# Kernel optimization log

Measured on AMD Instinct MI355X. Metric: run time of the kernel, lower is better.

The kernel has to match this reference:

```python
import jax, jax.numpy as jnp
import numpy as np

T, B, NINP, NHID, NOUT = 512, 256, 128, 512, 64


def setup_inputs() -> dict:
    key = jax.random.key(0)
    ks = jax.random.split(key, 8)
    s = 0.05
    return {
        "input": jax.random.normal(ks[0], (T, B, NINP - 1), dtype=jnp.float32),
        "dt": jax.random.uniform(ks[1], (T, B, 1), dtype=jnp.float32),
        "W_ih": jax.random.normal(ks[2], (4 * NHID, NINP), dtype=jnp.float32) * s,
        "W_hh": jax.random.normal(ks[3], (4 * NHID, NHID), dtype=jnp.float32) * s,
        "b_ih": jax.random.normal(ks[4], (4 * NHID,), dtype=jnp.float32) * s,
        "b_hh": jax.random.normal(ks[5], (4 * NHID,), dtype=jnp.float32) * s,
        "W_cls": jax.random.normal(ks[6], (NOUT, NHID), dtype=jnp.float32) * s,
        "b_cls": jax.random.normal(ks[7], (NOUT,), dtype=jnp.float32) * s,
    }


def reference(input, dt, W_ih, W_hh, b_ih, b_hh, W_cls, b_cls):
    # x_t = cat(inp_t, dt_t) -> [T, B, NINP]
    x = jnp.concatenate([input, dt], axis=-1)
    nhid = W_hh.shape[1]
    # Precompute input projections for all steps: [T, B, 4*nhid]
    x_proj = jnp.einsum("tbi,gi->tbg", x, W_ih) + b_ih + b_hh

    def step(carry, xp_t):
        h, c = carry
        gates = xp_t + h @ W_hh.T  # [B, 4*nhid]
        i, f, g, o = jnp.split(gates, 4, axis=-1)  # PyTorch LSTMCell gate order
        i = jax.nn.sigmoid(i)
        f = jax.nn.sigmoid(f)
        g = jnp.tanh(g)
        o = jax.nn.sigmoid(o)
        c = f * c + i * g
        h = o * jnp.tanh(c)
        return (h, c), h

    h0 = jnp.zeros((x.shape[1], nhid), dtype=x.dtype)
    c0 = jnp.zeros((x.shape[1], nhid), dtype=x.dtype)
    _, hs = jax.lax.scan(step, (h0, c0), x_proj)  # hs: [T, B, nhid]
    out = jnp.einsum("tbh,oh->tbo", hs, W_cls) + b_cls  # [T, B, nout]
    return out
```

## Files before the change

kernel.cpp:

```cpp
#include <hip/hip_runtime.h>
#include <stdint.h>

#define TT 512
#define BB 256
#define HH 512
#define NOUTC 64

typedef _Float16 f16;
typedef f16 f16x8 __attribute__((ext_vector_type(8)));
typedef float f32x4 __attribute__((ext_vector_type(4)));
typedef unsigned long long ull;

__device__ __forceinline__ float sigmoidf_(float x) {
  x = fminf(fmaxf(x, -30.f), 30.f);
  return 1.f / (1.f + __expf(-x));
}
__device__ __forceinline__ float tanhf_(float x) {
  x = fminf(fmaxf(x, -15.f), 15.f);
  float e = __expf(2.f * x);
  return (e - 1.f) / (e + 1.f);
}

__device__ __forceinline__ f16x8 cvt8(const float* __restrict__ src) {
  float4 p0 = *(const float4*)(src);
  float4 p1 = *(const float4*)(src + 4);
  f16x8 a;
  a[0] = (f16)p0.x; a[1] = (f16)p0.y; a[2] = (f16)p0.z; a[3] = (f16)p0.w;
  a[4] = (f16)p1.x; a[5] = (f16)p1.y; a[6] = (f16)p1.z; a[7] = (f16)p1.w;
  return a;
}

__global__ void zero_ws(uint32_t* __restrict__ ws, int nws) {
  int idx = blockIdx.x * blockDim.x + threadIdx.x;
  int stride = gridDim.x * blockDim.x;
  for (int i = idx; i < nws; i += stride) ws[i] = 0u;
}

__global__ __launch_bounds__(256, 1) void lstm_kernel(
    const float* __restrict__ input, const float* __restrict__ dtp,
    const float* __restrict__ W_ih, const float* __restrict__ W_hh,
    const float* __restrict__ b_ih, const float* __restrict__ b_hh,
    const float* __restrict__ W_cls, const float* __restrict__ b_cls,
    float* __restrict__ out, f16* __restrict__ h_buf) {
  __shared__ __align__(16) f16 xh_h[2][16][520];
  __shared__ __align__(16) f16 xb[2][16][136];
  __shared__ __align__(16) f16x8 wlds[16][64];

  const int tid = threadIdx.x;
  const int g = blockIdx.x & 15;
  const int s = blockIdx.x >> 4;
  const int b0 = g * 16;
  const int w = tid >> 6;
  const int lane = tid & 63;
  const int l = lane & 15;
  const int quad = lane >> 4;
  const int mt_o = s & 3;
  const bool cls_block = (s < 4);
  const int hb = s * 32 + w * 8;

  f16x8 afrag[2][20];
#pragma unroll
  for (int mp = 0; mp < 2; ++mp) {
    const int grow = (mp * 2 + (l >> 3)) * HH + hb + (l & 7);
#pragma unroll
    for (int it = 0; it < 20; ++it) {
      const int kb = it * 32 + quad * 8;
      const float* src = (kb < 128) ? (W_ih + (size_t)grow * 128 + kb)
                                    : (W_hh + (size_t)grow * HH + (kb - 128));
      afrag[mp][it] = cvt8(src);
    }
  }

  float gb_i[4], gb_f[4], gb_g[4], gb_o[4];
  {
    const int hg = hb + (quad & 1) * 4;
#pragma unroll
    for (int r = 0; r < 4; ++r) {
      gb_i[r] = b_ih[0 * HH + hg + r] + b_hh[0 * HH + hg + r];
      gb_f[r] = b_ih[1 * HH + hg + r] + b_hh[1 * HH + hg + r];
      gb_g[r] = b_ih[2 * HH + hg + r] + b_hh[2 * HH + hg + r];
      gb_o[r] = b_ih[3 * HH + hg + r] + b_hh[3 * HH + hg + r];
    }
  }

  float bcls4[4] = {0.f, 0.f, 0.f, 0.f};
  if (cls_block && w == 0) {
#pragma unroll
    for (int r = 0; r < 4; ++r) bcls4[r] = b_cls[mt_o * 16 + quad * 4 + r];
#pragma unroll
    for (int it = 0; it < 16; ++it)
      wlds[it][lane] =
          cvt8(W_cls + (size_t)(mt_o * 16 + l) * HH + it * 32 + quad * 8);
  }

  auto classify = [&](int slot, int tt) {
    f32x4 oa = {0.f, 0.f, 0.f, 0.f}, ob = {0.f, 0.f, 0.f, 0.f};
#pragma unroll
    for (int it = 0; it < 16; it += 2) {
      f16x8 ba = *(const f16x8*)(&xh_h[slot][l][it * 32 + quad * 8]);
      f16x8 bb = *(const f16x8*)(&xh_h[slot][l][(it + 1) * 32 + quad * 8]);
      oa = __builtin_amdgcn_mfma_f32_16x16x32_f16(wlds[it][lane], ba, oa, 0, 0, 0);
      ob = __builtin_amdgcn_mfma_f32_16x16x32_f16(wlds[it + 1][lane], bb, ob, 0, 0, 0);
    }
    float4 o;
    o.x = oa[0] + ob[0] + bcls4[0];
    o.y = oa[1] + ob[1] + bcls4[1];
    o.z = oa[2] + ob[2] + bcls4[2];
    o.w = oa[3] + ob[3] + bcls4[3];
    *(float4*)(out + ((size_t)tt * BB + b0 + l) * NOUTC + mt_o * 16 +
               quad * 4) = o;
  };

  auto stage_h = [&](int t_) {
    const uint32_t e = (uint32_t)((((t_ - 1) >> 1) & 1) ^ 1);
    const ull* hbp =
        (const ull*)h_buf + ((size_t)((t_ - 1) & 1) * 16 + g) * 2048;
    ull v[8];
#pragma unroll
    for (int ci = 0; ci < 8; ++ci)
      v[ci] = __hip_atomic_load(hbp + ci * 256 + tid, __ATOMIC_RELAXED,
                                __HIP_MEMORY_SCOPE_AGENT);
    for (int spin = 0; spin < (1 << 16); ++spin) {
      uint32_t stale = 0;
#pragma unroll
      for (int ci = 0; ci < 8; ++ci)
        if (((uint32_t)v[ci] ^ e) & 1u) stale |= 1u << ci;
      if (!stale) break;
      __builtin_amdgcn_s_sleep(1);
#pragma unroll
      for (int ci = 0; ci < 8; ++ci)
        if (stale & (1u << ci))
          v[ci] = __hip_atomic_load(hbp + ci * 256 + tid, __ATOMIC_RELAXED,
                                    __HIP_MEMORY_SCOPE_AGENT);
    }
#pragma unroll
    for (int ci = 0; ci < 8; ++ci) {
      const int c2 = ci * 256 + tid;
      *(ull*)(&xh_h[t_ & 1][c2 >> 7][(c2 & 127) * 4]) = v[ci];
    }
  };

  {
    ull* zp = (ull*)&xh_h[0][0][0];
    for (int i = tid; i < 2080; i += 256) zp[i] = 0ull;
  }
  const int kx = tid & 127;
  const int nx0 = tid >> 7;
  float xf[8];
#pragma unroll
  for (int ii = 0; ii < 8; ++ii) {
    const int row = b0 + ii * 2 + nx0;
    xf[ii] = (kx < 127) ? input[(size_t)row * 127 + kx] : dtp[row];
  }
  float cc[4] = {0.f, 0.f, 0.f, 0.f};

  for (int t = 0; t < TT; ++t) {
    if (t > 0) stage_h(t);

#pragma unroll
    for (int ii = 0; ii < 8; ++ii) xb[t & 1][ii * 2 + nx0][kx] = (f16)xf[ii];

    __syncthreads();

    f32x4 acc0 = {0.f, 0.f, 0.f, 0.f}, acc1 = {0.f, 0.f, 0.f, 0.f};
    const int xs = t & 1;
#pragma unroll
    for (int it = 0; it < 4; ++it) {
      f16x8 b = *(const f16x8*)(&xb[xs][l][it * 32 + quad * 8]);
      acc0 = __builtin_amdgcn_mfma_f32_16x16x32_f16(afrag[0][it], b, acc0, 0, 0, 0);
      acc1 = __builtin_amdgcn_mfma_f32_16x16x32_f16(afrag[1][it], b, acc1, 0, 0, 0);
    }
#pragma unroll
    for (int kk = 0; kk < 16; ++kk) {
      f16x8 b = *(const f16x8*)(&xh_h[xs][l][kk * 32 + quad * 8]);
      acc0 = __builtin_amdgcn_mfma_f32_16x16x32_f16(afrag[0][4 + kk], b, acc0, 0, 0, 0);
      acc1 = __builtin_amdgcn_mfma_f32_16x16x32_f16(afrag[1][4 + kk], b, acc1, 0, 0, 0);
    }

    float fsh[4], osh[4];
#pragma unroll
    for (int r = 0; r < 4; ++r) {
      fsh[r] = __shfl_xor(acc0[r], 32, 64);
      osh[r] = __shfl_xor(acc1[r], 32, 64);
    }
    if (quad < 2) {
      union { f16 h4[4]; ull u; } pk;
#pragma unroll
      for (int r = 0; r < 4; ++r) {
        float vi = acc0[r] + gb_i[r];
        float vf = fsh[r] + gb_f[r];
        float vg = acc1[r] + gb_g[r];
        float vo = osh[r] + gb_o[r];
        float iv = sigmoidf_(vi), fv = sigmoidf_(vf);
        float gv = tanhf_(vg), ov = sigmoidf_(vo);
        cc[r] = fv * cc[r] + iv * gv;
        pk.h4[r] = (f16)(ov * tanhf_(cc[r]));
      }
      pk.u = (pk.u & ~1ull) | (ull)((((t >> 1) & 1) ^ 1));
      __hip_atomic_store(
          (ull*)(h_buf + ((size_t)(t & 1) * 16 + g) * (16 * HH) +
                 (size_t)l * HH + hb + quad * 4),
          pk.u, __ATOMIC_RELAXED, __HIP_MEMORY_SCOPE_AGENT);
    }
    asm volatile("" ::: "memory");

    if (t + 1 < TT) {
#pragma unroll
      for (int ii = 0; ii < 8; ++ii) {
        const int row = (t + 1) * BB + b0 + ii * 2 + nx0;
        xf[ii] = (kx < 127) ? input[(size_t)row * 127 + kx] : dtp[row];
      }
    }

    if (t > 0 && cls_block && w == 0) classify(t & 1, t - 1);
  }

  if (cls_block) {
    stage_h(TT);
    __syncthreads();
    if (w == 0) classify(0, TT - 1);
  }
}

extern "C" void kernel_launch(void* const* d_in, const int* in_sizes, int n_in,
                              void* d_out, int out_size, void* d_ws,
                              size_t ws_size, hipStream_t stream) {
  const float* input = (const float*)d_in[0];
  const float* dtp = (const float*)d_in[1];
  const float* W_ih = (const float*)d_in[2];
  const float* W_hh = (const float*)d_in[3];
  const float* b_ih = (const float*)d_in[4];
  const float* b_hh = (const float*)d_in[5];
  const float* W_cls = (const float*)d_in[6];
  const float* b_cls = (const float*)d_in[7];
  float* out = (float*)d_out;

  f16* h_buf = (f16*)d_ws;
  const int nws_words = (2 * 16 * 16 * HH * 2) / 4;

  zero_ws<<<256, 256, 0, stream>>>((uint32_t*)d_ws, nws_words);
  lstm_kernel<<<256, 256, 0, stream>>>(input, dtp, W_ih, W_hh, b_ih, b_hh,
                                       W_cls, b_cls, out, h_buf);
}
```

Baseline: 1.761 ms.

## Restructure LSTM step loop to overlap h polling, x prefetch and classify

Reorders the per-timestep schedule. The next step's h loads are issued right after the current h store, and the x staging and classifier MFMAs run while those loads are in flight. The x input is prefetched two steps ahead, and the gate MFMA chain is split across two accumulator pairs to shorten dependency latency. The goal is to hide cross-block polling latency and MFMA dependency stalls on the serial critical path, at the cost of extra registers and a more delicate buffer-slot ordering.

```diff
diff --git a/kernel.cpp b/kernel.cpp
--- a/kernel.cpp
+++ b/kernel.cpp
@@ -111,71 +111,60 @@
                quad * 4) = o;
   };
 
-  auto stage_h = [&](int t_) {
-    const uint32_t e = (uint32_t)((((t_ - 1) >> 1) & 1) ^ 1);
-    const ull* hbp =
-        (const ull*)h_buf + ((size_t)((t_ - 1) & 1) * 16 + g) * 2048;
-    ull v[8];
-#pragma unroll
-    for (int ci = 0; ci < 8; ++ci)
-      v[ci] = __hip_atomic_load(hbp + ci * 256 + tid, __ATOMIC_RELAXED,
-                                __HIP_MEMORY_SCOPE_AGENT);
-    for (int spin = 0; spin < (1 << 16); ++spin) {
-      uint32_t stale = 0;
-#pragma unroll
-      for (int ci = 0; ci < 8; ++ci)
-        if (((uint32_t)v[ci] ^ e) & 1u) stale |= 1u << ci;
-      if (!stale) break;
-      __builtin_amdgcn_s_sleep(1);
-#pragma unroll
-      for (int ci = 0; ci < 8; ++ci)
-        if (stale & (1u << ci))
-          v[ci] = __hip_atomic_load(hbp + ci * 256 + tid, __ATOMIC_RELAXED,
-                                    __HIP_MEMORY_SCOPE_AGENT);
-    }
-#pragma unroll
-    for (int ci = 0; ci < 8; ++ci) {
-      const int c2 = ci * 256 + tid;
-      *(ull*)(&xh_h[t_ & 1][c2 >> 7][(c2 & 127) * 4]) = v[ci];
-    }
-  };
-
   {
     ull* zp = (ull*)&xh_h[0][0][0];
     for (int i = tid; i < 2080; i += 256) zp[i] = 0ull;
   }
   const int kx = tid & 127;
   const int nx0 = tid >> 7;
-  float xf[8];
 #pragma unroll
   for (int ii = 0; ii < 8; ++ii) {
     const int row = b0 + ii * 2 + nx0;
+    float v = (kx < 127) ? input[(size_t)row * 127 + kx] : dtp[row];
+    xb[0][ii * 2 + nx0][kx] = (f16)v;
+  }
+  float xf[8];
+#pragma unroll
+  for (int ii = 0; ii < 8; ++ii) {
+    const int row = BB + b0 + ii * 2 + nx0;
     xf[ii] = (kx < 127) ? input[(size_t)row * 127 + kx] : dtp[row];
   }
   float cc[4] = {0.f, 0.f, 0.f, 0.f};
+  __syncthreads();
 
   for (int t = 0; t < TT; ++t) {
-    if (t > 0) stage_h(t);
-
-#pragma unroll
-    for (int ii = 0; ii < 8; ++ii) xb[t & 1][ii * 2 + nx0][kx] = (f16)xf[ii];
-
-    __syncthreads();
-
-    f32x4 acc0 = {0.f, 0.f, 0.f, 0.f}, acc1 = {0.f, 0.f, 0.f, 0.f};
     const int xs = t & 1;
-#pragma unroll
-    for (int it = 0; it < 4; ++it) {
-      f16x8 b = *(const f16x8*)(&xb[xs][l][it * 32 + quad * 8]);
-      acc0 = __builtin_amdgcn_mfma_f32_16x16x32_f16(afrag[0][it], b, acc0, 0, 0, 0);
-      acc1 = __builtin_amdgcn_mfma_f32_16x16x32_f16(afrag[1][it], b, acc1, 0, 0, 0);
-    }
-#pragma unroll
-    for (int kk = 0; kk < 16; ++kk) {
-      f16x8 b = *(const f16x8*)(&xh_h[xs][l][kk * 32 + quad * 8]);
-      acc0 = __builtin_amdgcn_mfma_f32_16x16x32_f16(afrag[0][4 + kk], b, acc0, 0, 0, 0);
-      acc1 = __builtin_amdgcn_mfma_f32_16x16x32_f16(afrag[1][4 + kk], b, acc1, 0, 0, 0);
-    }
+
+    float xf2[8];
+    if (t + 2 < TT) {
+#pragma unroll
+      for (int ii = 0; ii < 8; ++ii) {
+        const int row = (t + 2) * BB + b0 + ii * 2 + nx0;
+        xf2[ii] = (kx < 127) ? input[(size_t)row * 127 + kx] : dtp[row];
+      }
+    }
+
+    f32x4 a0a = {0.f, 0.f, 0.f, 0.f}, a0b = {0.f, 0.f, 0.f, 0.f};
+    f32x4 a1a = {0.f, 0.f, 0.f, 0.f}, a1b = {0.f, 0.f, 0.f, 0.f};
+#pragma unroll
+    for (int it = 0; it < 4; it += 2) {
+      f16x8 b0f = *(const f16x8*)(&xb[xs][l][it * 32 + quad * 8]);
+      f16x8 b1f = *(const f16x8*)(&xb[xs][l][(it + 1) * 32 + quad * 8]);
+      a0a = __builtin_amdgcn_mfma_f32_16x16x32_f16(afrag[0][it], b0f, a0a, 0, 0, 0);
+      a1a = __builtin_amdgcn_mfma_f32_16x16x32_f16(afrag[1][it], b0f, a1a, 0, 0, 0);
+      a0b = __builtin_amdgcn_mfma_f32_16x16x32_f16(afrag[0][it + 1], b1f, a0b, 0, 0, 0);
+      a1b = __builtin_amdgcn_mfma_f32_16x16x32_f16(afrag[1][it + 1], b1f, a1b, 0, 0, 0);
+    }
+#pragma unroll
+    for (int kk = 0; kk < 16; kk += 2) {
+      f16x8 b0f = *(const f16x8*)(&xh_h[xs][l][kk * 32 + quad * 8]);
+      f16x8 b1f = *(const f16x8*)(&xh_h[xs][l][(kk + 1) * 32 + quad * 8]);
+      a0a = __builtin_amdgcn_mfma_f32_16x16x32_f16(afrag[0][4 + kk], b0f, a0a, 0, 0, 0);
+      a1a = __builtin_amdgcn_mfma_f32_16x16x32_f16(afrag[1][4 + kk], b0f, a1a, 0, 0, 0);
+      a0b = __builtin_amdgcn_mfma_f32_16x16x32_f16(afrag[0][5 + kk], b1f, a0b, 0, 0, 0);
+      a1b = __builtin_amdgcn_mfma_f32_16x16x32_f16(afrag[1][5 + kk], b1f, a1b, 0, 0, 0);
+    }
+    f32x4 acc0 = a0a + a0b, acc1 = a1a + a1b;
 
     float fsh[4], osh[4];
 #pragma unroll
@@ -204,22 +193,51 @@
     }
     asm volatile("" ::: "memory");
 
+    const ull* hbp = (const ull*)h_buf + ((size_t)(t & 1) * 16 + g) * 2048;
+    ull v[8];
+#pragma unroll
+    for (int ci = 0; ci < 8; ++ci)
+      v[ci] = __hip_atomic_load(hbp + ci * 256 + tid, __ATOMIC_RELAXED,
+                                __HIP_MEMORY_SCOPE_AGENT);
+
     if (t + 1 < TT) {
 #pragma unroll
-      for (int ii = 0; ii < 8; ++ii) {
-        const int row = (t + 1) * BB + b0 + ii * 2 + nx0;
-        xf[ii] = (kx < 127) ? input[(size_t)row * 127 + kx] : dtp[row];
-      }
-    }
-
-    if (t > 0 && cls_block && w == 0) classify(t & 1, t - 1);
-  }
-
-  if (cls_block) {
-    stage_h(TT);
+      for (int ii = 0; ii < 8; ++ii)
+        xb[xs ^ 1][ii * 2 + nx0][kx] = (f16)xf[ii];
+    }
+    if (t > 0 && cls_block && w == 0) classify(xs, t - 1);
+
+    {
+      const uint32_t e = (uint32_t)((((t >> 1) & 1) ^ 1));
+      for (int spin = 0; spin < (1 << 16); ++spin) {
+        uint32_t stale = 0;
+#pragma unroll
+        for (int ci = 0; ci < 8; ++ci)
+          if (((uint32_t)v[ci] ^ e) & 1u) stale |= 1u << ci;
+        if (!stale) break;
+        __builtin_amdgcn_s_sleep(1);
+#pragma unroll
+        for (int ci = 0; ci < 8; ++ci)
+          if (stale & (1u << ci))
+            v[ci] = __hip_atomic_load(hbp + ci * 256 + tid, __ATOMIC_RELAXED,
+                                      __HIP_MEMORY_SCOPE_AGENT);
+      }
+#pragma unroll
+      for (int ci = 0; ci < 8; ++ci) {
+        const int c2 = ci * 256 + tid;
+        *(ull*)(&xh_h[xs ^ 1][c2 >> 7][(c2 & 127) * 4]) = v[ci];
+      }
+    }
+
+    if (t + 2 < TT) {
+#pragma unroll
+      for (int ii = 0; ii < 8; ++ii) xf[ii] = xf2[ii];
+    }
+
     __syncthreads();
-    if (w == 0) classify(0, TT - 1);
-  }
+  }
+
+  if (cls_block && w == 0) classify(0, TT - 1);
 }
 
 extern "C" void kernel_launch(void* const* d_in, const int* in_sizes, int n_in,
```

Measured after the change: 3.322 ms. +88.6%, slower.
